# Kernel tuning notes

Hardware: AMD Instinct MI355X
Metric: run time of the kernel (lower is better)

Reference implementation:

```python
import jax, jax.numpy as jnp
import numpy as np

NUM_NODES = 50000
NUM_RELS = 47        # 2*23 + 1 after enrich()
EMB_DIM = 1600
WEIGHTS_SIZE = 16
NUM_CLASSES = 50
BASES = 40
NUM_EDGES = 1600000


def setup_inputs() -> dict:
    key = jax.random.key(0)
    ks = jax.random.split(key, 8)
    return {
        "node_embeddings": jax.random.normal(ks[0], (NUM_NODES, EMB_DIM), jnp.float32),
        "comps1": jax.random.normal(ks[1], (NUM_RELS, BASES), jnp.float32),
        "bases1": jax.random.normal(ks[2], (BASES, EMB_DIM, WEIGHTS_SIZE), jnp.float32) * 0.05,
        "comps2": jax.random.normal(ks[3], (NUM_RELS, BASES), jnp.float32),
        "bases2": jax.random.normal(ks[4], (BASES, WEIGHTS_SIZE, NUM_CLASSES), jnp.float32) * 0.05,
        "bias1": jnp.zeros((WEIGHTS_SIZE,), jnp.float32),
        "bias2": jnp.zeros((NUM_CLASSES,), jnp.float32),
        "rows": jax.random.randint(ks[5], (NUM_EDGES,), 0, NUM_NODES, jnp.int32),
        "cols": jax.random.randint(ks[6], (NUM_EDGES,), 0, NUM_RELS * NUM_NODES, jnp.int32),
    }


def _spmm(rows, cols, vals, h_rel):
    # hor_graph @ h_rel : h_rel is (R*N, d); out[n] = sum_e vals[e] * h_rel[cols[e]]
    msgs = vals[:, None] * h_rel[cols]              # (E, d)
    return jax.ops.segment_sum(msgs, rows, num_segments=NUM_NODES)


def reference(node_embeddings, comps1, bases1, comps2, bases2, bias1, bias2, rows, cols):
    R, N = NUM_RELS, NUM_NODES
    # normalization: 1 / row-sums of vertical adjacency == 1 / counts per hor column
    cnt = jax.ops.segment_sum(jnp.ones_like(cols, jnp.float32), cols, num_segments=R * N)
    vals = 1.0 / cnt[cols]                          # (E,)

    # layer 1: basis-decomposed per-relation transform
    w1 = jnp.einsum('rb,bio->rio', comps1, bases1)  # (R, emb, ws)
    h = jnp.einsum('ni,rio->rno', node_embeddings, w1)  # (R, N, ws)
    h = h.reshape(R * N, WEIGHTS_SIZE)
    h = _spmm(rows, cols, vals, h)                  # (N, ws)
    h = jax.nn.relu(h + bias1)

    # layer 2
    w2 = jnp.einsum('rb,bio->rio', comps2, bases2)  # (R, ws, C)
    h = jnp.einsum('ni,rio->rno', h, w2)            # (R, N, C)
    h = h.reshape(R * N, NUM_CLASSES)
    h = _spmm(rows, cols, vals, h)                  # (N, C)
    return h + bias2
```

## Files before the change

kernel.cpp:

```cpp
#include <hip/hip_runtime.h>
#include <hip/hip_bf16.h>

#define NN 50000
#define RR 47
#define ED 1600
#define WS 16
#define NC 50
#define NB 40
#define NE 1600000
#define WJ (RR*WS)
#define WJP 768

typedef unsigned short ushort_t;
typedef short s16x8 __attribute__((ext_vector_type(8)));
typedef float f32x4 __attribute__((ext_vector_type(4)));

__device__ __forceinline__ ushort_t f2bf(float f) {
    __hip_bfloat16 h = __float2bfloat16(f);
    ushort_t u;
    __builtin_memcpy(&u, &h, 2);
    return u;
}
__device__ __forceinline__ float bf2f(ushort_t u) {
    unsigned v = ((unsigned)u) << 16;
    float f;
    __builtin_memcpy(&f, &v, 4);
    return f;
}

__device__ __forceinline__ void async_copy16(const ushort_t* g, ushort_t* l) {
    __builtin_amdgcn_global_load_lds(
        (const __attribute__((address_space(1))) unsigned int*)g,
        (__attribute__((address_space(3))) unsigned int*)l,
        16, 0, 0);
}

__global__ void cast_kernel(const float* __restrict__ X, ushort_t* __restrict__ A) {
    int idx = blockIdx.x * blockDim.x + threadIdx.x;
    if (idx >= (NN * ED) / 4) return;
    float4 v = ((const float4*)X)[idx];
    ushort_t* p = &A[idx * 4];
    p[0] = f2bf(v.x); p[1] = f2bf(v.y); p[2] = f2bf(v.z); p[3] = f2bf(v.w);
}

__global__ void count_kernel(const int* __restrict__ cols, float* __restrict__ cnt) {
    int e = blockIdx.x * blockDim.x + threadIdx.x;
    if (e < NE) atomicAdd(&cnt[cols[e]], 1.0f);
}

__global__ void wbigbt_kernel(const float* __restrict__ comps1, const float* __restrict__ bases1,
                              ushort_t* __restrict__ WbigB) {
    int idx = blockIdx.x * blockDim.x + threadIdx.x;
    if (idx >= WJP * ED) return;
    int j = idx / ED;
    int i = idx - j * ED;
    float s = 0.f;
    if (j < WJ) {
        int r = j >> 4;
        int o = j & 15;
#pragma unroll
        for (int b = 0; b < NB; ++b)
            s += comps1[r * NB + b] * bases1[(b * ED + i) * WS + o];
    }
    WbigB[idx] = f2bf(s);
}

__global__ __launch_bounds__(256) void mfma_gemm_kernel(const ushort_t* __restrict__ A,
                                                        const ushort_t* __restrict__ B,
                                                        ushort_t* __restrict__ C) {
    __shared__ ushort_t Abuf[128 * 32];
    __shared__ ushort_t Bbuf[128 * 32];

    const int t = threadIdx.x;
    const int lane = t & 63;
    const int wave = t >> 6;
    const int m0 = blockIdx.x * 128;
    const int n0 = blockIdx.y * 128;
    const int wm = (wave & 1) * 64;
    const int wn = (wave >> 1) * 64;

    const int arow0 = t >> 2,        akp0 = (t & 3) * 8;
    const int arow1 = (t + 256) >> 2, akp1 = ((t + 256) & 3) * 8;
    int gm0 = m0 + arow0; if (gm0 >= NN) gm0 = NN - 1;
    int gm1 = m0 + arow1; if (gm1 >= NN) gm1 = NN - 1;
    const ushort_t* ap0 = &A[(size_t)gm0 * ED + akp0];
    const ushort_t* ap1 = &A[(size_t)gm1 * ED + akp1];
    const ushort_t* bp0 = &B[(size_t)(n0 + arow0) * ED + akp0];
    const ushort_t* bp1 = &B[(size_t)(n0 + arow1) * ED + akp1];

    f32x4 acc[4][4];
#pragma unroll
    for (int i = 0; i < 4; ++i)
#pragma unroll
        for (int j = 0; j < 4; ++j) acc[i][j] = (f32x4){0.f, 0.f, 0.f, 0.f};

    const int frow = lane & 15;
    const int fk = (lane >> 4) * 8;

    for (int k0 = 0; k0 < ED; k0 += 32) {
        async_copy16(ap0 + k0, &Abuf[t * 8]);
        async_copy16(ap1 + k0, &Abuf[(t + 256) * 8]);
        async_copy16(bp0 + k0, &Bbuf[t * 8]);
        async_copy16(bp1 + k0, &Bbuf[(t + 256) * 8]);
        __syncthreads();

        s16x8 af[4], bf[4];
#pragma unroll
        for (int mt = 0; mt < 4; ++mt)
            af[mt] = *(const s16x8*)&Abuf[(wm + mt * 16 + frow) * 32 + fk];
#pragma unroll
        for (int nt = 0; nt < 4; ++nt)
            bf[nt] = *(const s16x8*)&Bbuf[(wn + nt * 16 + frow) * 32 + fk];
#pragma unroll
        for (int mt = 0; mt < 4; ++mt)
#pragma unroll
            for (int nt = 0; nt < 4; ++nt)
                acc[mt][nt] = __builtin_amdgcn_mfma_f32_16x16x32_bf16(af[mt], bf[nt], acc[mt][nt], 0, 0, 0);
        __syncthreads();
    }

    const int cm = (lane >> 4) * 4;
    const int cn = lane & 15;
#pragma unroll
    for (int mt = 0; mt < 4; ++mt) {
#pragma unroll
        for (int i = 0; i < 4; ++i) {
            int gm = m0 + wm + mt * 16 + cm + i;
            if (gm >= NN) continue;
#pragma unroll
            for (int nt = 0; nt < 4; ++nt) {
                int gn = n0 + wn + nt * 16 + cn;
                if (gn < WJ) C[(size_t)gm * WJ + gn] = f2bf(acc[mt][nt][i]);
            }
        }
    }
}

__global__ void spmm1_kernel(const int* __restrict__ rows, const int* __restrict__ cols,
                             const float* __restrict__ cnt, const ushort_t* __restrict__ hrel,
                             float* __restrict__ h1) {
    int tid = blockIdx.x * blockDim.x + threadIdx.x;
    int e = tid >> 4;
    if (e >= NE) return;
    int o = tid & 15;
    int col = cols[e];
    int row = rows[e];
    float v = 1.0f / cnt[col];
    int r = col / NN;
    int n = col - r * NN;
    float x = bf2f(hrel[(size_t)n * WJ + r * WS + o]);
    atomicAdd(&h1[row * WS + o], v * x);
}

__global__ void relu_kernel(float* __restrict__ h1, const float* __restrict__ bias1) {
    int idx = blockIdx.x * blockDim.x + threadIdx.x;
    if (idx >= NN * WS) return;
    float v = h1[idx] + bias1[idx & 15];
    h1[idx] = v > 0.f ? v : 0.f;
}

__global__ void w2p_kernel(const float* __restrict__ comps2, const float* __restrict__ bases2,
                           float* __restrict__ w2p) {
    int idx = blockIdx.x * blockDim.x + threadIdx.x;
    if (idx >= WJ * 64) return;
    int k = idx >> 6;
    int c = idx & 63;
    float s = 0.f;
    if (c < NC) {
        int r = k >> 4;
        int o = k & 15;
#pragma unroll
        for (int b = 0; b < NB; ++b)
            s += comps2[r * NB + b] * bases2[(b * WS + o) * NC + c];
    }
    w2p[idx] = s;
}

__global__ void agg_kernel(const int* __restrict__ rows, const int* __restrict__ cols,
                           const float* __restrict__ cnt, const float* __restrict__ h1,
                           float* __restrict__ G) {
    int tid = blockIdx.x * blockDim.x + threadIdx.x;
    int e = tid >> 4;
    if (e >= NE) return;
    int o = tid & 15;
    int col = cols[e];
    int row = rows[e];
    float v = 1.0f / cnt[col];
    int r = col / NN;
    int n = col - r * NN;
    float x = h1[n * WS + o];
    atomicAdd(&G[(size_t)row * WJ + r * WS + o], v * x);
}

__global__ __launch_bounds__(256) void gemm2_kernel(const float* __restrict__ G,
                                                    const float* __restrict__ w2p,
                                                    const float* __restrict__ bias2,
                                                    float* __restrict__ out) {
    __shared__ float As[16][64];
    __shared__ float Bs[16][64 + 4];

    int t = threadIdx.x;
    int m0 = blockIdx.x * 64;
    int tx = t & 15, ty = t >> 4;

    float acc[4][4] = {};

    int arow = t >> 2, ak = (t & 3) * 4;
    int bk = t >> 4, bn = (t & 15) * 4;

    for (int k0 = 0; k0 < WJ; k0 += 16) {
        {
            int gm = m0 + arow;
            float4 av = make_float4(0.f, 0.f, 0.f, 0.f);
            if (gm < NN) av = *(const float4*)&G[(size_t)gm * WJ + k0 + ak];
            As[ak + 0][arow] = av.x;
            As[ak + 1][arow] = av.y;
            As[ak + 2][arow] = av.z;
            As[ak + 3][arow] = av.w;
        }
        {
            float4 bv = *(const float4*)&w2p[(k0 + bk) * 64 + bn];
            *(float4*)&Bs[bk][bn] = bv;
        }
        __syncthreads();
#pragma unroll
        for (int k = 0; k < 16; ++k) {
            float4 a = *(const float4*)&As[k][ty * 4];
            float4 b = *(const float4*)&Bs[k][tx * 4];
            float av[4] = {a.x, a.y, a.z, a.w};
            float bv[4] = {b.x, b.y, b.z, b.w};
#pragma unroll
            for (int i = 0; i < 4; ++i)
#pragma unroll
                for (int j = 0; j < 4; ++j)
                    acc[i][j] += av[i] * bv[j];
        }
        __syncthreads();
    }

#pragma unroll
    for (int i = 0; i < 4; ++i) {
        int gm = m0 + ty * 4 + i;
        if (gm >= NN) break;
#pragma unroll
        for (int j = 0; j < 4; ++j) {
            int gn = tx * 4 + j;
            if (gn < NC) out[gm * NC + gn] = acc[i][j] + bias2[gn];
        }
    }
}

extern "C" void kernel_launch(void* const* d_in, const int* in_sizes, int n_in,
                              void* d_out, int out_size, void* d_ws, size_t ws_size,
                              hipStream_t stream) {
    const float* X      = (const float*)d_in[0];
    const float* comps1 = (const float*)d_in[1];
    const float* bases1 = (const float*)d_in[2];
    const float* comps2 = (const float*)d_in[3];
    const float* bases2 = (const float*)d_in[4];
    const float* bias1  = (const float*)d_in[5];
    const float* bias2  = (const float*)d_in[6];
    const int*   rows   = (const int*)d_in[7];
    const int*   cols   = (const int*)d_in[8];
    float* out = (float*)d_out;

    char* ws = (char*)d_ws;
    float*    cnt   = (float*)   (ws + 0);
    ushort_t* Abf   = (ushort_t*)(ws + 9400064);
    float*    G     = (float*)   (ws + 9400064);
    ushort_t* WbigB = (ushort_t*)(ws + 169400064);
    ushort_t* hrel  = (ushort_t*)(ws + 171857664);
    float*    h1    = (float*)   (ws + 247057664);
    float*    w2p   = (float*)   (ws + 250257664);

    hipMemsetAsync(cnt, 0, (size_t)RR * NN * 4, stream);
    hipMemsetAsync(h1, 0, (size_t)NN * WS * 4, stream);

    cast_kernel<<<(NN * ED / 4 + 255) / 256, 256, 0, stream>>>(X, Abf);
    count_kernel<<<(NE + 255) / 256, 256, 0, stream>>>(cols, cnt);
    wbigbt_kernel<<<(WJP * ED + 255) / 256, 256, 0, stream>>>(comps1, bases1, WbigB);

    dim3 ggrid((NN + 127) / 128, WJP / 128);
    mfma_gemm_kernel<<<ggrid, 256, 0, stream>>>(Abf, WbigB, hrel);

    spmm1_kernel<<<(NE * 16) / 256, 256, 0, stream>>>(rows, cols, cnt, hrel, h1);
    relu_kernel<<<(NN * WS + 255) / 256, 256, 0, stream>>>(h1, bias1);
    w2p_kernel<<<(WJ * 64 + 255) / 256, 256, 0, stream>>>(comps2, bases2, w2p);

    hipMemsetAsync(G, 0, (size_t)NN * WJ * 4, stream);
    agg_kernel<<<(NE * 16) / 256, 256, 0, stream>>>(rows, cols, cnt, h1, G);

    gemm2_kernel<<<(NN + 63) / 64, 256, 0, stream>>>(G, w2p, bias2, out);
}
```

Baseline: 1.105 ms.

## Build CSR by row and fuse layer-2 aggregation with GEMM in shared memory

Builds a row-sorted CSR (histogram, three-stage scan, scatter) so layer 1 becomes a per-row gather reduction with fused bias and ReLU, with no global atomics. Layer 2 accumulates each row block's relation-expanded features into shared memory and multiplies by W2 in the same kernel. This removes the 160 MB dense G buffer, its memset and the global atomics into it. The MFMA GEMM grid is also remapped so consecutive tiles stay on the same XCD for L2 reuse. The cost is extra preprocessing kernels, LDS atomics, and a one-row-per-thread layer-2 GEMM with low reuse.

```diff
diff --git a/kernel.cpp b/kernel.cpp
--- a/kernel.cpp
+++ b/kernel.cpp
@@ -10,6 +10,11 @@
 #define NE 1600000
 #define WJ (RR*WS)
 #define WJP 768
+
+#define GEMM_NBLK 2346
+#define SCAN_B 1024
+#define SCAN_NBLK ((NN + SCAN_B - 1) / SCAN_B)
+#define L2ROWS 16
 
 typedef unsigned short ushort_t;
 typedef short s16x8 __attribute__((ext_vector_type(8)));
@@ -71,11 +76,18 @@
     __shared__ ushort_t Abuf[128 * 32];
     __shared__ ushort_t Bbuf[128 * 32];
 
+    const int bid = blockIdx.x;
+    const int q = GEMM_NBLK / 8, rm = GEMM_NBLK % 8;
+    const int xcd = bid & 7, loc = bid >> 3;
+    const int sbid = (xcd < rm ? xcd * (q + 1) : rm * (q + 1) + (xcd - rm) * q) + loc;
+    const int mb = sbid / 6;
+    const int nb = sbid - mb * 6;
+
     const int t = threadIdx.x;
     const int lane = t & 63;
     const int wave = t >> 6;
-    const int m0 = blockIdx.x * 128;
-    const int n0 = blockIdx.y * 128;
+    const int m0 = mb * 128;
+    const int n0 = nb * 128;
     const int wm = (wave & 1) * 64;
     const int wn = (wave >> 1) * 64;
 
@@ -136,27 +148,84 @@
     }
 }
 
-__global__ void spmm1_kernel(const int* __restrict__ rows, const int* __restrict__ cols,
-                             const float* __restrict__ cnt, const ushort_t* __restrict__ hrel,
-                             float* __restrict__ h1) {
-    int tid = blockIdx.x * blockDim.x + threadIdx.x;
-    int e = tid >> 4;
+__global__ void hist_kernel(const int* __restrict__ rows, int* __restrict__ rcnt) {
+    int e = blockIdx.x * blockDim.x + threadIdx.x;
+    if (e < NE) atomicAdd(&rcnt[rows[e]], 1);
+}
+
+__global__ __launch_bounds__(SCAN_B) void scan1_kernel(const int* __restrict__ rcnt,
+                                                       int* __restrict__ ptr,
+                                                       int* __restrict__ bsum) {
+    __shared__ int buf[2][SCAN_B];
+    int t = threadIdx.x, base = blockIdx.x * SCAN_B;
+    int v = (base + t < NN) ? rcnt[base + t] : 0;
+    buf[0][t] = v;
+    __syncthreads();
+    int src = 0;
+    for (int off = 1; off < SCAN_B; off <<= 1) {
+        int x = buf[src][t];
+        if (t >= off) x += buf[src][t - off];
+        buf[src ^ 1][t] = x;
+        src ^= 1;
+        __syncthreads();
+    }
+    int incl = buf[src][t];
+    if (base + t < NN) ptr[base + t] = incl - v;
+    if (t == SCAN_B - 1) bsum[blockIdx.x] = incl;
+}
+
+__global__ void scan2_kernel(int* __restrict__ bsum, int* __restrict__ ptr) {
+    if (threadIdx.x == 0 && blockIdx.x == 0) {
+        int run = 0;
+        for (int i = 0; i < SCAN_NBLK; ++i) { int v = bsum[i]; bsum[i] = run; run += v; }
+        ptr[NN] = run;
+    }
+}
+
+__global__ void scan3_kernel(const int* __restrict__ bsum, int* __restrict__ ptr) {
+    int idx = blockIdx.x * blockDim.x + threadIdx.x;
+    if (idx < NN) ptr[idx] += bsum[idx >> 10];
+}
+
+__global__ void scatter_kernel(const int* __restrict__ rows, const int* __restrict__ cols,
+                               const float* __restrict__ cnt, const int* __restrict__ ptr,
+                               int* __restrict__ fill, int* __restrict__ ecol,
+                               float* __restrict__ eval) {
+    int e = blockIdx.x * blockDim.x + threadIdx.x;
     if (e >= NE) return;
-    int o = tid & 15;
-    int col = cols[e];
-    int row = rows[e];
-    float v = 1.0f / cnt[col];
-    int r = col / NN;
-    int n = col - r * NN;
-    float x = bf2f(hrel[(size_t)n * WJ + r * WS + o]);
-    atomicAdd(&h1[row * WS + o], v * x);
-}
-
-__global__ void relu_kernel(float* __restrict__ h1, const float* __restrict__ bias1) {
-    int idx = blockIdx.x * blockDim.x + threadIdx.x;
-    if (idx >= NN * WS) return;
-    float v = h1[idx] + bias1[idx & 15];
-    h1[idx] = v > 0.f ? v : 0.f;
+    int rw = rows[e];
+    int pos = ptr[rw] + atomicAdd(&fill[rw], 1);
+    int c = cols[e];
+    ecol[pos] = c;
+    eval[pos] = 1.0f / cnt[c];
+}
+
+__global__ __launch_bounds__(256) void spmm1_csr_kernel(const int* __restrict__ ptr,
+        const int* __restrict__ ecol, const float* __restrict__ eval,
+        const ushort_t* __restrict__ hrel, const float* __restrict__ bias1,
+        float* __restrict__ h1) {
+    int t = threadIdx.x;
+    int wave = t >> 6, lane = t & 63;
+    int m = blockIdx.x * 4 + wave;
+    int start = ptr[m], end = ptr[m + 1];
+    int o = lane & 15, sub = lane >> 4;
+    float acc = 0.f;
+    for (int e0 = start; e0 < end; e0 += 4) {
+        int e = e0 + sub;
+        if (e < end) {
+            int col = ecol[e];
+            float v = eval[e];
+            int r = col / NN;
+            int n = col - r * NN;
+            acc += v * bf2f(hrel[(size_t)n * WJ + r * WS + o]);
+        }
+    }
+    acc += __shfl_xor(acc, 16);
+    acc += __shfl_xor(acc, 32);
+    if (lane < 16) {
+        float hv = acc + bias1[o];
+        h1[m * WS + o] = hv > 0.f ? hv : 0.f;
+    }
 }
 
 __global__ void w2p_kernel(const float* __restrict__ comps2, const float* __restrict__ bases2,
@@ -176,76 +245,58 @@
     w2p[idx] = s;
 }
 
-__global__ void agg_kernel(const int* __restrict__ rows, const int* __restrict__ cols,
-                           const float* __restrict__ cnt, const float* __restrict__ h1,
-                           float* __restrict__ G) {
-    int tid = blockIdx.x * blockDim.x + threadIdx.x;
-    int e = tid >> 4;
-    if (e >= NE) return;
-    int o = tid & 15;
-    int col = cols[e];
-    int row = rows[e];
-    float v = 1.0f / cnt[col];
-    int r = col / NN;
-    int n = col - r * NN;
-    float x = h1[n * WS + o];
-    atomicAdd(&G[(size_t)row * WJ + r * WS + o], v * x);
-}
-
-__global__ __launch_bounds__(256) void gemm2_kernel(const float* __restrict__ G,
-                                                    const float* __restrict__ w2p,
-                                                    const float* __restrict__ bias2,
-                                                    float* __restrict__ out) {
-    __shared__ float As[16][64];
-    __shared__ float Bs[16][64 + 4];
+__global__ __launch_bounds__(256) void layer2_kernel(const int* __restrict__ ptr,
+        const int* __restrict__ ecol, const float* __restrict__ eval,
+        const float* __restrict__ h1, const float* __restrict__ w2p,
+        const float* __restrict__ bias2, float* __restrict__ out) {
+    __shared__ float gt[L2ROWS][WJ];
+    __shared__ float Bs[16][68];
 
     int t = threadIdx.x;
-    int m0 = blockIdx.x * 64;
-    int tx = t & 15, ty = t >> 4;
-
-    float acc[4][4] = {};
-
-    int arow = t >> 2, ak = (t & 3) * 4;
-    int bk = t >> 4, bn = (t & 15) * 4;
-
+    int m0 = blockIdx.x * L2ROWS;
+
+    for (int i = t; i < L2ROWS * WJ; i += 256) ((float*)gt)[i] = 0.f;
+    __syncthreads();
+
+    int wave = t >> 6, lane = t & 63;
+    int o = lane & 15, sub = lane >> 4;
+    for (int lr = wave * 4; lr < wave * 4 + 4; ++lr) {
+        int m = m0 + lr;
+        if (m >= NN) break;
+        int start = ptr[m], end = ptr[m + 1];
+        for (int e0 = start; e0 < end; e0 += 4) {
+            int e = e0 + sub;
+            if (e < end) {
+                int col = ecol[e];
+                float v = eval[e];
+                int r = col / NN;
+                int n = col - r * NN;
+                atomicAdd(&gt[lr][r * WS + o], v * h1[n * WS + o]);
+            }
+        }
+    }
+    __syncthreads();
+
+    int i = t >> 4, tx = t & 15;
+    float acc[4] = {0.f, 0.f, 0.f, 0.f};
     for (int k0 = 0; k0 < WJ; k0 += 16) {
-        {
-            int gm = m0 + arow;
-            float4 av = make_float4(0.f, 0.f, 0.f, 0.f);
-            if (gm < NN) av = *(const float4*)&G[(size_t)gm * WJ + k0 + ak];
-            As[ak + 0][arow] = av.x;
-            As[ak + 1][arow] = av.y;
-            As[ak + 2][arow] = av.z;
-            As[ak + 3][arow] = av.w;
-        }
-        {
-            float4 bv = *(const float4*)&w2p[(k0 + bk) * 64 + bn];
-            *(float4*)&Bs[bk][bn] = bv;
-        }
+        *(float4*)&Bs[t >> 4][(t & 15) * 4] =
+            *(const float4*)&w2p[(k0 + (t >> 4)) * 64 + (t & 15) * 4];
         __syncthreads();
 #pragma unroll
         for (int k = 0; k < 16; ++k) {
-            float4 a = *(const float4*)&As[k][ty * 4];
+            float a = gt[i][k0 + k];
             float4 b = *(const float4*)&Bs[k][tx * 4];
-            float av[4] = {a.x, a.y, a.z, a.w};
-            float bv[4] = {b.x, b.y, b.z, b.w};
-#pragma unroll
-            for (int i = 0; i < 4; ++i)
-#pragma unroll
-                for (int j = 0; j < 4; ++j)
-                    acc[i][j] += av[i] * bv[j];
-        }
-        __syncthreads();
-    }
-
-#pragma unroll
-    for (int i = 0; i < 4; ++i) {
-        int gm = m0 + ty * 4 + i;
-        if (gm >= NN) break;
+            acc[0] += a * b.x; acc[1] += a * b.y; acc[2] += a * b.z; acc[3] += a * b.w;
+        }
+        __syncthreads();
+    }
+    int m = m0 + i;
+    if (m < NN) {
 #pragma unroll
         for (int j = 0; j < 4; ++j) {
-            int gn = tx * 4 + j;
-            if (gn < NC) out[gm * NC + gn] = acc[i][j] + bias2[gn];
+            int c = tx * 4 + j;
+            if (c < NC) out[m * NC + c] = acc[j] + bias2[c];
         }
     }
 }
@@ -265,30 +316,37 @@
     float* out = (float*)d_out;
 
     char* ws = (char*)d_ws;
-    float*    cnt   = (float*)   (ws + 0);
-    ushort_t* Abf   = (ushort_t*)(ws + 9400064);
-    float*    G     = (float*)   (ws + 9400064);
-    ushort_t* WbigB = (ushort_t*)(ws + 169400064);
-    ushort_t* hrel  = (ushort_t*)(ws + 171857664);
-    float*    h1    = (float*)   (ws + 247057664);
-    float*    w2p   = (float*)   (ws + 250257664);
+    float*    cnt    = (float*)   (ws + 0);
+    ushort_t* Abf    = (ushort_t*)(ws + 9400064);
+    int*      rowptr = (int*)     (ws + 9400064);
+    int*      rcnt   = (int*)     (ws + 9600128);
+    int*      fill   = (int*)     (ws + 9800192);
+    int*      bsum   = (int*)     (ws + 10000256);
+    int*      ecol   = (int*)     (ws + 10000512);
+    float*    eval   = (float*)   (ws + 16400512);
+    ushort_t* WbigB  = (ushort_t*)(ws + 169400064);
+    ushort_t* hrel   = (ushort_t*)(ws + 171857664);
+    float*    h1     = (float*)   (ws + 247057664);
+    float*    w2p    = (float*)   (ws + 250257664);
 
     hipMemsetAsync(cnt, 0, (size_t)RR * NN * 4, stream);
-    hipMemsetAsync(h1, 0, (size_t)NN * WS * 4, stream);
 
     cast_kernel<<<(NN * ED / 4 + 255) / 256, 256, 0, stream>>>(X, Abf);
     count_kernel<<<(NE + 255) / 256, 256, 0, stream>>>(cols, cnt);
     wbigbt_kernel<<<(WJP * ED + 255) / 256, 256, 0, stream>>>(comps1, bases1, WbigB);
 
-    dim3 ggrid((NN + 127) / 128, WJP / 128);
-    mfma_gemm_kernel<<<ggrid, 256, 0, stream>>>(Abf, WbigB, hrel);
-
-    spmm1_kernel<<<(NE * 16) / 256, 256, 0, stream>>>(rows, cols, cnt, hrel, h1);
-    relu_kernel<<<(NN * WS + 255) / 256, 256, 0, stream>>>(h1, bias1);
+    mfma_gemm_kernel<<<GEMM_NBLK, 256, 0, stream>>>(Abf, WbigB, hrel);
+
+    hipMemsetAsync(rcnt, 0, (size_t)NN * 4, stream);
+    hipMemsetAsync(fill, 0, (size_t)NN * 4, stream);
+    hist_kernel<<<(NE + 255) / 256, 256, 0, stream>>>(rows, rcnt);
+    scan1_kernel<<<SCAN_NBLK, SCAN_B, 0, stream>>>(rcnt, rowptr, bsum);
+    scan2_kernel<<<1, 64, 0, stream>>>(bsum, rowptr);
+    scan3_kernel<<<(NN + 255) / 256, 256, 0, stream>>>(bsum, rowptr);
+    scatter_kernel<<<(NE + 255) / 256, 256, 0, stream>>>(rows, cols, cnt, rowptr, fill, ecol, eval);
+
+    spmm1_csr_kernel<<<NN / 4, 256, 0, stream>>>(rowptr, ecol, eval, hrel, bias1, h1);
+
     w2p_kernel<<<(WJ * 64 + 255) / 256, 256, 0, stream>>>(comps2, bases2, w2p);
-
-    hipMemsetAsync(G, 0, (size_t)NN * WJ * 4, stream);
-    agg_kernel<<<(NE * 16) / 256, 256, 0, stream>>>(rows, cols, cnt, h1, G);
-
-    gemm2_kernel<<<(NN + 63) / 64, 256, 0, stream>>>(G, w2p, bias2, out);
-}
+    layer2_kernel<<<(NN + L2ROWS - 1) / L2ROWS, 256, 0, stream>>>(rowptr, ecol, eval, h1, w2p, bias2, out);
+}
```

Result: slower. 1.321 ms (+19.5%).
